# Kernel tuning notes

Hardware: AMD Instinct MI355X
Metric: run time of the kernel (lower is better)

Reference implementation:

```python
import jax, jax.numpy as jnp
import numpy as np

DK = 128
B, S = 16, 2048

def setup_inputs() -> dict:
    key = jax.random.key(0)
    kq, kk, kv = jax.random.split(key, 3)
    q = jax.random.normal(kq, (B, S, DK), dtype=jnp.float32)
    k = jax.random.normal(kk, (B, S, DK), dtype=jnp.float32)
    v = jax.random.normal(kv, (B, S, DK), dtype=jnp.float32)
    return {"q": q, "k": k, "v": v}

def reference(q, k, v):
    # scores: [B, S, S]
    scale = 1.0 / jnp.sqrt(jnp.float32(DK))
    scores = jnp.einsum("bqd,bkd->bqk", q, k) * scale
    probs = jax.nn.softmax(scores, axis=-1)
    # dropout is identity in eval mode (training=None)
    return jnp.einsum("bqk,bkd->bqd", probs, v)
```

## Files before the change

kernel.cpp:

```cpp
#include <hip/hip_runtime.h>
#include <hip/hip_bf16.h>

#define BATCH 16
#define SEQ   2048
#define DK    128
#define NT    16
#define SC2   0.12751744f
#define THRL2 11.541560f

typedef __attribute__((ext_vector_type(8)))  short short8v;
typedef __attribute__((ext_vector_type(4)))  float float4v;
typedef __attribute__((ext_vector_type(16))) float float16v;

typedef const __attribute__((address_space(1))) unsigned int* gas_t;
typedef __attribute__((address_space(3))) unsigned int* las_t;

__device__ inline void gl_lds16(const void* g, void* l) {
    __builtin_amdgcn_global_load_lds((gas_t)g, (las_t)l, 16, 0, 0);
}

__device__ inline short f2bf(float f) {
    __hip_bfloat16 h = __float2bfloat16(f);
    unsigned short u;
    __builtin_memcpy(&u, &h, sizeof(u));
    return (short)u;
}

__device__ inline unsigned cvt_pk_bf16(float a, float b) {
    unsigned r;
    asm("v_cvt_pk_bf16_f32 %0, %1, %2" : "=v"(r) : "v"(a), "v"(b));
    return r;
}

__global__ __launch_bounds__(256)
void prepass_kernel(const float* __restrict__ k, const float* __restrict__ v,
                    short* __restrict__ kb, short* __restrict__ vt)
{
    if (blockIdx.x < 2048) {
        size_t i = ((size_t)blockIdx.x * 256 + threadIdx.x) * 8;
        float4 a = *reinterpret_cast<const float4*>(k + i);
        float4 b = *reinterpret_cast<const float4*>(k + i + 4);
        short8v t;
        t[0] = f2bf(a.x * SC2); t[1] = f2bf(a.y * SC2); t[2] = f2bf(a.z * SC2); t[3] = f2bf(a.w * SC2);
        t[4] = f2bf(b.x * SC2); t[5] = f2bf(b.y * SC2); t[6] = f2bf(b.z * SC2); t[7] = f2bf(b.w * SC2);
        *reinterpret_cast<short8v*>(kb + i) = t;
        return;
    }

    __shared__ float tile[32][33];
    const int vb_ = blockIdx.x - 2048;
    const int b   = vb_ >> 8;
    const int st  = (vb_ >> 2) & 63;
    const int dt  = vb_ & 3;
    const int s0  = st * 32;
    const int d0  = dt * 32;

    const int tx = threadIdx.x & 31;
    const int ty = threadIdx.x >> 5;
    const float* vbp = v + ((size_t)b * SEQ + s0) * DK + d0;
#pragma unroll
    for (int i = 0; i < 4; ++i) {
        int r = ty + 8 * i;
        tile[r][tx] = vbp[(size_t)r * DK + tx];
    }
    __syncthreads();

    const int d  = threadIdx.x >> 3;
    const int g2 = (threadIdx.x >> 2) & 1;
    const int qq = threadIdx.x & 3;
    const int kvb = g2 * 16 + ((qq >> 1) << 2) + ((qq & 1) << 3);

    const float f0 = tile[kvb + 0][d];
    const float f1 = tile[kvb + 1][d];
    const float f2 = tile[kvb + 2][d];
    const float f3 = tile[kvb + 3][d];
    union { unsigned u[2]; unsigned long long ll; } pk;
    pk.u[0] = cvt_pk_bf16(f0, f1);
    pk.u[1] = cvt_pk_bf16(f2, f3);

    short* o = vt + ((size_t)b * DK + d0 + d) * SEQ + s0 + g2 * 16 + qq * 4;
    *reinterpret_cast<unsigned long long*>(o) = pk.ll;
}

__global__ __launch_bounds__(512, 2)
void attn_fwd_v18(const float* __restrict__ q,
                  const short* __restrict__ kb,
                  const short* __restrict__ vt,
                  float* __restrict__ out)
{
    __shared__ __align__(16) char lds[131072];

    const int tid  = threadIdx.x;
    const int lane = tid & 63;
    const int wave = tid >> 6;
    const int qt   = wave & 3;
    const int h    = wave >> 2;
    const int bid  = blockIdx.x;
    const int work = (bid & 7) * 32 + (bid >> 3);
    const int b    = work >> 4;
    const int q0   = (work & 15) * 128 + qt * 32;

    const int l31 = lane & 31;
    const int hi  = lane >> 5;

    const float* qrow = q + ((size_t)b * SEQ + q0 + l31) * DK + hi * 8;
    short8v qf[8];
#pragma unroll
    for (int s = 0; s < 8; ++s) {
        float4 x = *reinterpret_cast<const float4*>(qrow + s * 16);
        float4 y = *reinterpret_cast<const float4*>(qrow + s * 16 + 4);
        union { unsigned u[4]; short8v v; } pk;
        pk.u[0] = cvt_pk_bf16(x.x, x.y);
        pk.u[1] = cvt_pk_bf16(x.z, x.w);
        pk.u[2] = cvt_pk_bf16(y.x, y.y);
        pk.u[3] = cvt_pk_bf16(y.z, y.w);
        qf[s] = pk.v;
    }

    const char* kB = (const char*)(kb + (size_t)b * SEQ * DK);
    const char* vB = (const char*)(vt + (size_t)b * DK * SEQ);
    const int hkv = h * 1024;

    const char* src[8];
    int dstoff[8];
    long sstep;
    if (qt < 2) {
#pragma unroll
        for (int i = 0; i < 8; ++i) {
            const int kr = qt * 32 + i * 4 + (lane >> 4);
            src[i] = kB + (size_t)(hkv + kr) * 256 + (((lane & 15) ^ (kr & 15)) << 4);
            dstoff[i] = h * 32768 + qt * 8192 + i * 1024;
        }
        sstep = 64 * 256;
    } else {
#pragma unroll
        for (int i = 0; i < 8; ++i) {
            const int R  = (qt - 2) * 32 + i * 4 + (lane >> 4);
            const int wx = (lane & 15) ^ (R & 15);
            const int d  = 2 * R + (wx >> 3);
            src[i] = vB + (size_t)d * (SEQ * 2) + (size_t)hkv * 2 + ((wx & 7) << 4);
            dstoff[i] = h * 32768 + 16384 + (qt - 2) * 8192 + i * 1024;
        }
        sstep = 64 * 2;
    }

    float m_run = -1e30f;
    float l_run = 0.0f;
    float16v o[4];
#pragma unroll
    for (int dblk = 0; dblk < 4; ++dblk)
#pragma unroll
        for (int i = 0; i < 16; ++i) o[dblk][i] = 0.f;

    auto STAGE = [&](int bufsel, int t) {
        char* base = lds + bufsel * 65536;
#pragma unroll
        for (int i = 0; i < 8; ++i)
            gl_lds16(src[i] + (size_t)t * sstep, base + dstoff[i]);
    };

    STAGE(0, 0);
    __syncthreads();

    int buf = 0;
    for (int t = 0; t < NT; ++t) {
        if (t + 1 < NT) STAGE(buf ^ 1, t + 1);

        const char* Kl = lds + buf * 65536 + h * 32768;
        const char* Vl = Kl + 16384;
        const char* ka = Kl + l31 * 256;

        float16v sa[2];
#pragma unroll
        for (int i = 0; i < 16; ++i) { sa[0][i] = 0.f; sa[1][i] = 0.f; }
        __builtin_amdgcn_s_setprio(1);
#pragma unroll
        for (int s = 0; s < 8; ++s) {
            const int un = ((2 * s + hi) ^ (l31 & 15)) << 4;
            short8v kf0 = *reinterpret_cast<const short8v*>(ka + un);
            short8v kf1 = *reinterpret_cast<const short8v*>(ka + 8192 + un);
            sa[0] = __builtin_amdgcn_mfma_f32_32x32x16_bf16(kf0, qf[s], sa[0], 0, 0, 0);
            sa[1] = __builtin_amdgcn_mfma_f32_32x32x16_bf16(kf1, qf[s], sa[1], 0, 0, 0);
        }
        __builtin_amdgcn_s_setprio(0);

        float t16[16];
#pragma unroll
        for (int i = 0; i < 16; ++i) t16[i] = fmaxf(sa[0][i], sa[1][i]);
#pragma unroll
        for (int s2 = 8; s2 > 0; s2 >>= 1)
#pragma unroll
            for (int i = 0; i < s2; ++i) t16[i] = fmaxf(t16[i], t16[i + s2]);
        float mx = fmaxf(t16[0], __shfl_xor(t16[0], 32));

        if (!__all(mx <= m_run + THRL2)) {
            const float mnew  = fmaxf(m_run, mx);
            const float alpha = exp2f(m_run - mnew);
            l_run *= alpha;
            m_run = mnew;
            float aq[16];
#pragma unroll
            for (int reg = 0; reg < 16; ++reg)
                aq[reg] = __shfl(alpha, (reg & 3) + 8 * (reg >> 2) + 4 * hi);
#pragma unroll
            for (int dblk = 0; dblk < 4; ++dblk)
#pragma unroll
                for (int reg = 0; reg < 16; ++reg) o[dblk][reg] *= aq[reg];
        }

        float ts4[4] = {0.f, 0.f, 0.f, 0.f};
#pragma unroll
        for (int sub = 0; sub < 2; ++sub)
#pragma unroll
            for (int i = 0; i < 16; ++i) {
                const float e = exp2f(sa[sub][i] - m_run);
                sa[sub][i] = e;
                ts4[i & 3] += e;
            }
        float ts = (ts4[0] + ts4[1]) + (ts4[2] + ts4[3]);
        ts += __shfl_xor(ts, 32);
        l_run += ts;

        short8v pf[4];
#pragma unroll
        for (int g = 0; g < 4; ++g) {
            const int sub = g >> 1, r0 = (g & 1) * 8;
            union { unsigned u[4]; short8v v; } pk;
            pk.u[0] = cvt_pk_bf16(sa[sub][r0 + 0], sa[sub][r0 + 1]);
            pk.u[1] = cvt_pk_bf16(sa[sub][r0 + 2], sa[sub][r0 + 3]);
            pk.u[2] = cvt_pk_bf16(sa[sub][r0 + 4], sa[sub][r0 + 5]);
            pk.u[3] = cvt_pk_bf16(sa[sub][r0 + 6], sa[sub][r0 + 7]);
            pf[g] = pk.v;
        }

        __builtin_amdgcn_s_setprio(1);
#pragma unroll
        for (int dblk = 0; dblk < 4; ++dblk) {
            const int R  = dblk * 16 + (l31 >> 1);
            const char* vr = Vl + R * 256;
            const int dh = (l31 & 1) << 3;
#pragma unroll
            for (int g = 0; g < 4; ++g) {
                const int w = ((dh | (2 * g + hi)) ^ (R & 15)) << 4;
                short8v vf = *reinterpret_cast<const short8v*>(vr + w);
                o[dblk] = __builtin_amdgcn_mfma_f32_32x32x16_bf16(pf[g], vf, o[dblk], 0, 0, 0);
            }
        }
        __builtin_amdgcn_s_setprio(0);

        __syncthreads();
        buf ^= 1;
    }

    float* smO = (float*)lds;
    float* smM = (float*)(lds + 65536);
    float* smL = (float*)(lds + 66048);

    if (h == 1) {
        if (hi == 0) { smM[qt * 32 + l31] = m_run; smL[qt * 32 + l31] = l_run; }
#pragma unroll
        for (int dblk = 0; dblk < 4; ++dblk)
#pragma unroll
            for (int reg = 0; reg < 16; ++reg) {
                const int qp = (reg & 3) + 8 * (reg >> 2) + 4 * hi;
                smO[(qt * 32 + qp) * 128 + dblk * 32 + l31] = o[dblk][reg];
            }
    }
    __syncthreads();
    if (h == 0) {
        const float m1 = smM[qt * 32 + l31];
        const float l1 = smL[qt * 32 + l31];
        const float mf = fmaxf(m_run, m1);
        const float a0 = exp2f(m_run - mf);
        const float a1 = exp2f(m1 - mf);
        const float li = 1.0f / (l_run * a0 + l1 * a1);
        const float w0 = a0 * li;
        const float w1 = a1 * li;

        float w0q[16], w1q[16];
#pragma unroll
        for (int reg = 0; reg < 16; ++reg) {
            const int qp = (reg & 3) + 8 * (reg >> 2) + 4 * hi;
            w0q[reg] = __shfl(w0, qp);
            w1q[reg] = __shfl(w1, qp);
        }

        float* ob = out + ((size_t)b * SEQ + q0) * DK;
#pragma unroll
        for (int dblk = 0; dblk < 4; ++dblk)
#pragma unroll
            for (int reg = 0; reg < 16; ++reg) {
                const int qp = (reg & 3) + 8 * (reg >> 2) + 4 * hi;
                ob[(size_t)qp * DK + dblk * 32 + l31] =
                    o[dblk][reg] * w0q[reg]
                    + smO[(qt * 32 + qp) * 128 + dblk * 32 + l31] * w1q[reg];
            }
    }
}

__global__ __launch_bounds__(256)
void attn_fwd_slow(const float* __restrict__ q,
                   const float* __restrict__ k,
                   const float* __restrict__ v,
                   float* __restrict__ out)
{
    const int lane = threadIdx.x & 63;
    const int wave = threadIdx.x >> 6;
    const int b    = blockIdx.y;
    const int q0   = blockIdx.x * 64 + wave * 16;
    const int row = lane & 15;
    const int grp = lane >> 4;

    const float* qb = q + ((size_t)b * SEQ + q0) * DK;
    const float* kbp = k + (size_t)b * SEQ * DK;
    const float* vbp = v + (size_t)b * SEQ * DK;

    short8v qf[4];
#pragma unroll
    for (int c = 0; c < 4; ++c) {
        const float* p = qb + row * DK + c * 32 + grp * 8;
        float4 x = *reinterpret_cast<const float4*>(p);
        float4 y = *reinterpret_cast<const float4*>(p + 4);
        short8v t;
        t[0] = f2bf(x.x); t[1] = f2bf(x.y); t[2] = f2bf(x.z); t[3] = f2bf(x.w);
        t[4] = f2bf(y.x); t[5] = f2bf(y.y); t[6] = f2bf(y.z); t[7] = f2bf(y.w);
        qf[c] = t;
    }

    float m_run = -1e30f, l_run = 0.0f;
    float4v o[8];
#pragma unroll
    for (int i = 0; i < 8; ++i) { o[i][0]=0.f; o[i][1]=0.f; o[i][2]=0.f; o[i][3]=0.f; }
    const float scale = 0.08838834764831845f;

    for (int kv0 = 0; kv0 < SEQ; kv0 += 16) {
        short8v kf[4];
        const float* kp0 = kbp + (size_t)(kv0 + row) * DK + grp * 8;
#pragma unroll
        for (int c = 0; c < 4; ++c) {
            const float* p = kp0 + c * 32;
            float4 x = *reinterpret_cast<const float4*>(p);
            float4 y = *reinterpret_cast<const float4*>(p + 4);
            short8v t;
            t[0] = f2bf(x.x); t[1] = f2bf(x.y); t[2] = f2bf(x.z); t[3] = f2bf(x.w);
            t[4] = f2bf(y.x); t[5] = f2bf(y.y); t[6] = f2bf(y.z); t[7] = f2bf(y.w);
            kf[c] = t;
        }
        short8v vf[8];
#pragma unroll
        for (int dblk = 0; dblk < 8; ++dblk) {
            const float* p = vbp + (size_t)(kv0 + 4 * grp) * DK + dblk * 16 + row;
            short b0 = f2bf(p[0]);
            short b1 = f2bf(p[DK]);
            short b2 = f2bf(p[2 * DK]);
            short b3 = f2bf(p[3 * DK]);
            short8v t;
            t[0]=b0; t[1]=b1; t[2]=b2; t[3]=b3; t[4]=b0; t[5]=b1; t[6]=b2; t[7]=b3;
            vf[dblk] = t;
        }
        float4v s; s[0]=0.f; s[1]=0.f; s[2]=0.f; s[3]=0.f;
#pragma unroll
        for (int c = 0; c < 4; ++c)
            s = __builtin_amdgcn_mfma_f32_16x16x32_bf16(kf[c], qf[c], s, 0, 0, 0);

        float sv[4]; float tmax = -1e30f;
#pragma unroll
        for (int r = 0; r < 4; ++r) { sv[r] = s[r] * scale; tmax = fmaxf(tmax, sv[r]); }
        tmax = fmaxf(tmax, __shfl_xor(tmax, 16));
        tmax = fmaxf(tmax, __shfl_xor(tmax, 32));
        const float mnew = fmaxf(m_run, tmax);
        float pr[4]; float tsum = 0.f;
#pragma unroll
        for (int r = 0; r < 4; ++r) { pr[r] = __expf(sv[r] - mnew); tsum += pr[r]; }
        tsum += __shfl_xor(tsum, 16);
        tsum += __shfl_xor(tsum, 32);
        const float alpha = __expf(m_run - mnew);
        l_run = l_run * alpha + tsum;
        m_run = mnew;
        float aq[4];
#pragma unroll
        for (int r = 0; r < 4; ++r) aq[r] = __shfl(alpha, grp * 4 + r);
#pragma unroll
        for (int dblk = 0; dblk < 8; ++dblk)
#pragma unroll
            for (int r = 0; r < 4; ++r) o[dblk][r] *= aq[r];

        short8v pfv;
        pfv[0]=f2bf(pr[0]); pfv[1]=f2bf(pr[1]); pfv[2]=f2bf(pr[2]); pfv[3]=f2bf(pr[3]);
        pfv[4]=0; pfv[5]=0; pfv[6]=0; pfv[7]=0;
#pragma unroll
        for (int dblk = 0; dblk < 8; ++dblk)
            o[dblk] = __builtin_amdgcn_mfma_f32_16x16x32_bf16(pfv, vf[dblk], o[dblk], 0, 0, 0);
    }

    const float linv = 1.0f / l_run;
    float li[4];
#pragma unroll
    for (int r = 0; r < 4; ++r) li[r] = __shfl(linv, grp * 4 + r);
    float* ob = out + ((size_t)b * SEQ + q0) * DK;
#pragma unroll
    for (int dblk = 0; dblk < 8; ++dblk)
#pragma unroll
        for (int r = 0; r < 4; ++r)
            ob[(size_t)(grp * 4 + r) * DK + dblk * 16 + row] = o[dblk][r] * li[r];
}

extern "C" void kernel_launch(void* const* d_in, const int* in_sizes, int n_in,
                              void* d_out, int out_size, void* d_ws, size_t ws_size,
                              hipStream_t stream) {
    const float* q = (const float*)d_in[0];
    const float* k = (const float*)d_in[1];
    const float* v = (const float*)d_in[2];
    float* out = (float*)d_out;

    const size_t kb_bytes = (size_t)BATCH * SEQ * DK * sizeof(short);
    const size_t need = 2 * kb_bytes;

    if (ws_size >= need) {
        short* kbuf = (short*)d_ws;
        short* vtbuf = (short*)((char*)d_ws + kb_bytes);
        hipLaunchKernelGGL(prepass_kernel, dim3(2048 + 4096), dim3(256), 0, stream, k, v, kbuf, vtbuf);
        hipLaunchKernelGGL(attn_fwd_v18, dim3((SEQ / 128) * BATCH), dim3(512), 0, stream, q, kbuf, vtbuf, out);
    } else {
        hipLaunchKernelGGL(attn_fwd_slow, dim3(SEQ / 64, BATCH), dim3(256), 0, stream, q, k, v, out);
    }
}
```

Measured before the change: 63.66 us.

## Split KV tile into two 32-key halves with separate online-softmax steps

```diff
diff --git a/kernel.cpp b/kernel.cpp
--- a/kernel.cpp
+++ b/kernel.cpp
@@ -83,7 +83,7 @@
 }
 
 __global__ __launch_bounds__(512, 2)
-void attn_fwd_v18(const float* __restrict__ q,
+void attn_fwd_v19(const float* __restrict__ q,
                   const short* __restrict__ kb,
                   const short* __restrict__ vt,
                   float* __restrict__ out)
@@ -159,39 +159,15 @@
             gl_lds16(src[i] + (size_t)t * sstep, base + dstoff[i]);
     };
 
-    STAGE(0, 0);
-    __syncthreads();
-
-    int buf = 0;
-    for (int t = 0; t < NT; ++t) {
-        if (t + 1 < NT) STAGE(buf ^ 1, t + 1);
-
-        const char* Kl = lds + buf * 65536 + h * 32768;
-        const char* Vl = Kl + 16384;
-        const char* ka = Kl + l31 * 256;
-
-        float16v sa[2];
-#pragma unroll
-        for (int i = 0; i < 16; ++i) { sa[0][i] = 0.f; sa[1][i] = 0.f; }
-        __builtin_amdgcn_s_setprio(1);
-#pragma unroll
-        for (int s = 0; s < 8; ++s) {
-            const int un = ((2 * s + hi) ^ (l31 & 15)) << 4;
-            short8v kf0 = *reinterpret_cast<const short8v*>(ka + un);
-            short8v kf1 = *reinterpret_cast<const short8v*>(ka + 8192 + un);
-            sa[0] = __builtin_amdgcn_mfma_f32_32x32x16_bf16(kf0, qf[s], sa[0], 0, 0, 0);
-            sa[1] = __builtin_amdgcn_mfma_f32_32x32x16_bf16(kf1, qf[s], sa[1], 0, 0, 0);
-        }
-        __builtin_amdgcn_s_setprio(0);
-
-        float t16[16];
-#pragma unroll
-        for (int i = 0; i < 16; ++i) t16[i] = fmaxf(sa[0][i], sa[1][i]);
-#pragma unroll
-        for (int s2 = 8; s2 > 0; s2 >>= 1)
-#pragma unroll
-            for (int i = 0; i < s2; ++i) t16[i] = fmaxf(t16[i], t16[i + s2]);
-        float mx = fmaxf(t16[0], __shfl_xor(t16[0], 32));
+    auto SOFTMAX_SUB = [&](float16v& sa, short8v* pf) {
+        float t8[8];
+#pragma unroll
+        for (int i = 0; i < 8; ++i) t8[i] = fmaxf(sa[i], sa[i + 8]);
+#pragma unroll
+        for (int s2 = 4; s2 > 0; s2 >>= 1)
+#pragma unroll
+            for (int i = 0; i < s2; ++i) t8[i] = fmaxf(t8[i], t8[i + s2]);
+        const float mx = fmaxf(t8[0], __shfl_xor(t8[0], 32));
 
         if (!__all(mx <= m_run + THRL2)) {
             const float mnew  = fmaxf(m_run, mx);
@@ -210,28 +186,58 @@
 
         float ts4[4] = {0.f, 0.f, 0.f, 0.f};
 #pragma unroll
-        for (int sub = 0; sub < 2; ++sub)
-#pragma unroll
-            for (int i = 0; i < 16; ++i) {
-                const float e = exp2f(sa[sub][i] - m_run);
-                sa[sub][i] = e;
-                ts4[i & 3] += e;
-            }
+        for (int i = 0; i < 16; ++i) {
+            const float e = exp2f(sa[i] - m_run);
+            sa[i] = e;
+            ts4[i & 3] += e;
+        }
         float ts = (ts4[0] + ts4[1]) + (ts4[2] + ts4[3]);
         ts += __shfl_xor(ts, 32);
         l_run += ts;
 
-        short8v pf[4];
-#pragma unroll
-        for (int g = 0; g < 4; ++g) {
-            const int sub = g >> 1, r0 = (g & 1) * 8;
+#pragma unroll
+        for (int g = 0; g < 2; ++g) {
+            const int r0 = g * 8;
             union { unsigned u[4]; short8v v; } pk;
-            pk.u[0] = cvt_pk_bf16(sa[sub][r0 + 0], sa[sub][r0 + 1]);
-            pk.u[1] = cvt_pk_bf16(sa[sub][r0 + 2], sa[sub][r0 + 3]);
-            pk.u[2] = cvt_pk_bf16(sa[sub][r0 + 4], sa[sub][r0 + 5]);
-            pk.u[3] = cvt_pk_bf16(sa[sub][r0 + 6], sa[sub][r0 + 7]);
+            pk.u[0] = cvt_pk_bf16(sa[r0 + 0], sa[r0 + 1]);
+            pk.u[1] = cvt_pk_bf16(sa[r0 + 2], sa[r0 + 3]);
+            pk.u[2] = cvt_pk_bf16(sa[r0 + 4], sa[r0 + 5]);
+            pk.u[3] = cvt_pk_bf16(sa[r0 + 6], sa[r0 + 7]);
             pf[g] = pk.v;
         }
+    };
+
+    STAGE(0, 0);
+    __syncthreads();
+
+    int buf = 0;
+    for (int t = 0; t < NT; ++t) {
+        if (t + 1 < NT) STAGE(buf ^ 1, t + 1);
+
+        const char* Kl = lds + buf * 65536 + h * 32768;
+        const char* Vl = Kl + 16384;
+        const char* ka = Kl + l31 * 256;
+
+        float16v sa0, sa1;
+#pragma unroll
+        for (int i = 0; i < 16; ++i) { sa0[i] = 0.f; sa1[i] = 0.f; }
+        __builtin_amdgcn_s_setprio(1);
+#pragma unroll
+        for (int s = 0; s < 8; ++s) {
+            const int un = ((2 * s + hi) ^ (l31 & 15)) << 4;
+            short8v kf0 = *reinterpret_cast<const short8v*>(ka + un);
+            sa0 = __builtin_amdgcn_mfma_f32_32x32x16_bf16(kf0, qf[s], sa0, 0, 0, 0);
+        }
+#pragma unroll
+        for (int s = 0; s < 8; ++s) {
+            const int un = ((2 * s + hi) ^ (l31 & 15)) << 4;
+            short8v kf1 = *reinterpret_cast<const short8v*>(ka + 8192 + un);
+            sa1 = __builtin_amdgcn_mfma_f32_32x32x16_bf16(kf1, qf[s], sa1, 0, 0, 0);
+        }
+        __builtin_amdgcn_s_setprio(0);
+
+        short8v pf0[2];
+        SOFTMAX_SUB(sa0, pf0);
 
         __builtin_amdgcn_s_setprio(1);
 #pragma unroll
@@ -240,10 +246,28 @@
             const char* vr = Vl + R * 256;
             const int dh = (l31 & 1) << 3;
 #pragma unroll
-            for (int g = 0; g < 4; ++g) {
+            for (int g = 0; g < 2; ++g) {
                 const int w = ((dh | (2 * g + hi)) ^ (R & 15)) << 4;
                 short8v vf = *reinterpret_cast<const short8v*>(vr + w);
-                o[dblk] = __builtin_amdgcn_mfma_f32_32x32x16_bf16(pf[g], vf, o[dblk], 0, 0, 0);
+                o[dblk] = __builtin_amdgcn_mfma_f32_32x32x16_bf16(pf0[g], vf, o[dblk], 0, 0, 0);
+            }
+        }
+        __builtin_amdgcn_s_setprio(0);
+
+        short8v pf1[2];
+        SOFTMAX_SUB(sa1, pf1);
+
+        __builtin_amdgcn_s_setprio(1);
+#pragma unroll
+        for (int dblk = 0; dblk < 4; ++dblk) {
+            const int R  = dblk * 16 + (l31 >> 1);
+            const char* vr = Vl + R * 256;
+            const int dh = (l31 & 1) << 3;
+#pragma unroll
+            for (int g = 0; g < 2; ++g) {
+                const int w = ((dh | (2 * (g + 2) + hi)) ^ (R & 15)) << 4;
+                short8v vf = *reinterpret_cast<const short8v*>(vr + w);
+                o[dblk] = __builtin_amdgcn_mfma_f32_32x32x16_bf16(pf1[g], vf, o[dblk], 0, 0, 0);
             }
         }
         __builtin_amdgcn_s_setprio(0);
@@ -420,7 +444,7 @@
         short* kbuf = (short*)d_ws;
         short* vtbuf = (short*)((char*)d_ws + kb_bytes);
         hipLaunchKernelGGL(prepass_kernel, dim3(2048 + 4096), dim3(256), 0, stream, k, v, kbuf, vtbuf);
-        hipLaunchKernelGGL(attn_fwd_v18, dim3((SEQ / 128) * BATCH), dim3(512), 0, stream, q, kbuf, vtbuf, out);
+        hipLaunchKernelGGL(attn_fwd_v19, dim3((SEQ / 128) * BATCH), dim3(512), 0, stream, q, kbuf, vtbuf, out);
     } else {
         hipLaunchKernelGGL(attn_fwd_slow, dim3(SEQ / 64, BATCH), dim3(256), 0, stream, q, k, v, out);
     }
```

Measured after the change: 64.55 us. About the same (+1.4%).
